# Kernel optimization log

Measured on AMD Instinct MI355X. Metric: run time of the kernel, lower is better.

Reference implementation:

```python
import jax, jax.numpy as jnp
import numpy as np


def setup_inputs() -> dict:
    key = jax.random.key(0)
    ks = jax.random.split(key, 9)
    B, S, D, E, I = 4, 2048, 1024, 8, 2048
    sd = 1.0 / np.sqrt(D)
    si = 1.0 / np.sqrt(I)
    return {
        "hidden_states": jax.random.normal(ks[0], (B, S, D), dtype=jnp.float32),
        "gate_w": jax.random.normal(ks[1], (D, E), dtype=jnp.float32) * sd,
        "expert_gate_w": jax.random.normal(ks[2], (E, D, I), dtype=jnp.float32) * sd,
        "expert_up_w": jax.random.normal(ks[3], (E, D, I), dtype=jnp.float32) * sd,
        "expert_down_w": jax.random.normal(ks[4], (E, I, D), dtype=jnp.float32) * si,
        "shared_gate_proj_w": jax.random.normal(ks[5], (D, I), dtype=jnp.float32) * sd,
        "shared_up_w": jax.random.normal(ks[6], (D, I), dtype=jnp.float32) * sd,
        "shared_down_w": jax.random.normal(ks[7], (I, D), dtype=jnp.float32) * si,
        "shared_expert_gate_w": jax.random.normal(ks[8], (D, 1), dtype=jnp.float32) * sd,
        "top_k": 2,
    }


def reference(hidden_states, gate_w, expert_gate_w, expert_up_w, expert_down_w,
              shared_gate_proj_w, shared_up_w, shared_down_w, shared_expert_gate_w,
              top_k):
    B, S, D = hidden_states.shape
    E = gate_w.shape[1]
    x = hidden_states.reshape(-1, D)            # [T, D]
    T = x.shape[0]

    # Router: softmax in fp32, top-k, dense per-token per-expert combine weights.
    gate_vals = x @ gate_w                      # [T, E]
    probs = jax.nn.softmax(gate_vals.astype(jnp.float32), axis=-1)
    top_w, top_i = jax.lax.top_k(probs, top_k)  # [T, K]
    dense_w = jnp.zeros((T, E), dtype=jnp.float32)
    dense_w = dense_w.at[jnp.arange(T)[:, None], top_i].set(top_w)
    dense_w = dense_w.astype(x.dtype)           # zero for unselected experts

    # All experts as batched SwiGLU GEMMs (tokens with zero weight contribute 0).
    g = jnp.einsum('td,edi->eti', x, expert_gate_w)
    u = jnp.einsum('td,edi->eti', x, expert_up_w)
    y = jnp.einsum('eti,eid->etd', jax.nn.silu(g) * u, expert_down_w)  # [E, T, D]
    moe_out = jnp.einsum('etd,te->td', y, dense_w)                      # [T, D]

    # Shared expert with sigmoid gate.
    shared = (jax.nn.silu(x @ shared_gate_proj_w) * (x @ shared_up_w)) @ shared_down_w
    shared = jax.nn.sigmoid(x @ shared_expert_gate_w) * shared

    final = (moe_out + shared).reshape(B, S, D)
    return final, gate_vals
```

## Files before the change

kernel.cpp:

```cpp
#include <hip/hip_runtime.h>

typedef __bf16 bf16x8 __attribute__((ext_vector_type(8)));
typedef float f32x4 __attribute__((ext_vector_type(4)));
typedef float f4 __attribute__((ext_vector_type(4)));
typedef unsigned short us8 __attribute__((ext_vector_type(8)));

#define T_TOK 8192
#define DDIM 1024
#define NEXP 8
#define IDIM 2048
#define NCH 1024
#define RROWS 17408
#define ROWS_TOT (T_TOK + RROWS)

__device__ __forceinline__ unsigned short f2bf(float f) {
    unsigned u = __float_as_uint(f);
    u += 0x7fffu + ((u >> 16) & 1u);
    return (unsigned short)(u >> 16);
}

#define GLDS(src, dst) __builtin_amdgcn_global_load_lds( \
    (const __attribute__((address_space(1))) void*)(src), \
    (__attribute__((address_space(3))) void*)(dst), 16, 0, 0)

__global__ __launch_bounds__(256) void router_kernel(
    const float* __restrict__ x, const float* __restrict__ gate_w,
    const float* __restrict__ sgw, float* __restrict__ gate_out,
    float* __restrict__ wdense, float* __restrict__ sgout)
{
    __shared__ float lgw[DDIM * NEXP];
    __shared__ float lsg[DDIM];
    int tid = threadIdx.x;
    for (int i = tid; i < (DDIM * NEXP) / 4; i += 256)
        ((f4*)lgw)[i] = ((const f4*)gate_w)[i];
    for (int i = tid; i < DDIM / 4; i += 256)
        ((f4*)lsg)[i] = ((const f4*)sgw)[i];
    __syncthreads();

    int wid = tid >> 6, l = tid & 63;
    int t = blockIdx.x * 4 + wid;

    float acc[NEXP];
#pragma unroll
    for (int e = 0; e < NEXP; e++) acc[e] = 0.f;
    float accs = 0.f;
    const float* xr = x + (size_t)t * DDIM;
#pragma unroll
    for (int j = 0; j < 4; j++) {
        int d0 = j * 256 + l * 4;
        f4 xv = *(const f4*)(xr + d0);
#pragma unroll
        for (int c = 0; c < 4; c++) {
            float xd = xv[c];
            int d = d0 + c;
#pragma unroll
            for (int e = 0; e < NEXP; e++) acc[e] += xd * lgw[d * NEXP + e];
            accs += xd * lsg[d];
        }
    }
#pragma unroll
    for (int off = 32; off > 0; off >>= 1) {
#pragma unroll
        for (int e = 0; e < NEXP; e++) acc[e] += __shfl_xor(acc[e], off);
        accs += __shfl_xor(accs, off);
    }
    if (l == 0) {
        float m = acc[0];
        for (int e = 1; e < NEXP; e++) m = fmaxf(m, acc[e]);
        float p[NEXP], s = 0.f;
        for (int e = 0; e < NEXP; e++) { p[e] = __expf(acc[e] - m); s += p[e]; }
        float inv = 1.f / s;
        int i1 = 0; float b1 = p[0];
        for (int e = 1; e < NEXP; e++) if (p[e] > b1) { b1 = p[e]; i1 = e; }
        int i2 = -1; float b2 = -1.f;
        for (int e = 0; e < NEXP; e++) if (e != i1 && p[e] > b2) { b2 = p[e]; i2 = e; }
        for (int e = 0; e < NEXP; e++) {
            gate_out[(size_t)t * NEXP + e] = acc[e];
            float w = (e == i1) ? b1 * inv : (e == i2) ? b2 * inv : 0.f;
            wdense[(size_t)t * NEXP + e] = w;
        }
        sgout[t] = 1.f / (1.f + __expf(-accs));
    }
}

__global__ __launch_bounds__(256) void bucket_kernel(
    const float* __restrict__ wdense, int* __restrict__ list,
    float* __restrict__ wl, int* __restrict__ cnt,
    int* __restrict__ te, int* __restrict__ tp)
{
    int e = blockIdx.x;
    int tid = threadIdx.x, wid = tid >> 6, l = tid & 63;
    __shared__ int wsum[4];
    int base = 0;
    int* le = list + (size_t)e * T_TOK;
    float* we = wl + (size_t)e * T_TOK;
    for (int t0 = 0; t0 < T_TOK; t0 += 256) {
        int tok = t0 + tid;
        float w = wdense[(size_t)tok * NEXP + e];
        bool f = w > 0.f;
        unsigned long long m = __ballot(f);
        int lp = __popcll(m & ((1ull << l) - 1ull));
        if (l == 0) wsum[wid] = __popcll(m);
        __syncthreads();
        int woff = 0;
#pragma unroll
        for (int i = 0; i < 4; i++) if (i < wid) woff += wsum[i];
        int btot = wsum[0] + wsum[1] + wsum[2] + wsum[3];
        if (f) {
            int pos = base + woff + lp;
            le[pos] = tok; we[pos] = w;
            int slot = 0;
            for (int e2 = 0; e2 < e; e2++)
                slot += (wdense[(size_t)tok * NEXP + e2] > 0.f) ? 1 : 0;
            te[tok * 2 + slot] = e;
            tp[tok * 2 + slot] = pos;
        }
        base += btot;
        __syncthreads();
    }
    if (tid == 0) cnt[e] = base;
    int align = (base + 255) & ~255;
    for (int i = base + tid; i < align; i += 256) { le[i] = 0; we[i] = 0.f; }
}

__global__ void scan_kernel(const int* __restrict__ cnt, int* __restrict__ offs)
{
    if (threadIdx.x == 0) {
        int o = 0;
        for (int e = 0; e < NEXP; e++) { offs[e] = o; o += (cnt[e] + 127) & ~127; }
    }
}

__global__ __launch_bounds__(256) void cvt_kernel(
    const float* __restrict__ in, unsigned short* __restrict__ out, int n8)
{
    int i = blockIdx.x * 256 + threadIdx.x;
    if (i >= n8) return;
    const f4* p = (const f4*)in + (size_t)i * 2;
    f4 a = p[0], b = p[1];
    us8 o;
#pragma unroll
    for (int k = 0; k < 4; k++) { o[k] = f2bf(a[k]); o[4 + k] = f2bf(b[k]); }
    *((us8*)out + i) = o;
}

__global__ __launch_bounds__(256) void wcvt_gu_kernel(
    const float* __restrict__ egw, const float* __restrict__ euw,
    const float* __restrict__ sgp, const float* __restrict__ sup,
    unsigned short* __restrict__ pool, int c0)
{
    int j = blockIdx.y;
    int e = j >> 1, s = j & 1;
    const float* src = (e < 8) ? ((s ? euw : egw) + (size_t)e * DDIM * IDIM)
                               : (s ? sup : sgp);
    unsigned short* dst = pool + (size_t)j * NCH * DDIM;
    int tpc = NCH / 64;
    int tci = blockIdx.x % tpc, tri = blockIdx.x / tpc;
    int r0 = tri * 64;
    int cl0 = tci * 64;
    int cg0 = c0 + cl0;

    __shared__ unsigned short lds[64][72];
    int t = threadIdx.x;
    int tr = t >> 4, tcc = (t & 15) * 4;
#pragma unroll
    for (int jj = 0; jj < 4; jj++) {
        int r = tr + jj * 16;
        f4 v = *(const f4*)(src + (size_t)(r0 + r) * IDIM + cg0 + tcc);
#pragma unroll
        for (int k = 0; k < 4; k++) lds[r][tcc + k] = f2bf(v[k]);
    }
    __syncthreads();
    int orow = t >> 2, ss = t & 3;
    us8 v0, v1;
#pragma unroll
    for (int i = 0; i < 8; i++) {
        v0[i] = lds[ss * 16 + i][orow];
        v1[i] = lds[ss * 16 + 8 + i][orow];
    }
    unsigned short* op = dst + (size_t)(cl0 + orow) * DDIM + r0 + ss * 16;
    *(us8*)op = v0; *(us8*)(op + 8) = v1;
}

__global__ __launch_bounds__(256) void wcvt_d_kernel(
    const float* __restrict__ edw, const float* __restrict__ sdw,
    unsigned short* __restrict__ pool)
{
    int j = blockIdx.y;
    const float* src = (j < 8) ? edw + (size_t)j * IDIM * DDIM : sdw;
    unsigned short* dst = pool + (size_t)j * DDIM * IDIM;
    int tpc = DDIM / 64;
    int tci = blockIdx.x % tpc, tri = blockIdx.x / tpc;
    int rg0 = tri * 64;
    int cg0 = tci * 64;

    __shared__ unsigned short lds[64][72];
    int t = threadIdx.x;
    int tr = t >> 4, tcc = (t & 15) * 4;
#pragma unroll
    for (int jj = 0; jj < 4; jj++) {
        int r = tr + jj * 16;
        f4 v = *(const f4*)(src + (size_t)(rg0 + r) * DDIM + cg0 + tcc);
#pragma unroll
        for (int k = 0; k < 4; k++) lds[r][tcc + k] = f2bf(v[k]);
    }
    __syncthreads();
    int orow = t >> 2, ss = t & 3;
    us8 v0, v1;
#pragma unroll
    for (int i = 0; i < 8; i++) {
        v0[i] = lds[ss * 16 + i][orow];
        v1[i] = lds[ss * 16 + 8 + i][orow];
    }
    unsigned short* op = dst + (size_t)(cg0 + orow) * IDIM + rg0 + ss * 16;
    *(us8*)op = v0; *(us8*)(op + 8) = v1;
}

__global__ __launch_bounds__(512, 1) void gemm_gateup8(
    const unsigned short* __restrict__ A, const unsigned short* __restrict__ pool,
    unsigned short* __restrict__ H, const int* __restrict__ listb,
    const int* __restrict__ cnt, const int* __restrict__ offs, int c0)
{
    int z = blockIdx.z;
    const unsigned short *Bg, *Bu; const int* lst; int count, rowb;
    if (z == 0) {
        Bg = pool + (size_t)16 * NCH * DDIM; Bu = pool + (size_t)17 * NCH * DDIM;
        lst = nullptr; count = T_TOK; rowb = 0;
    } else {
        int e = z - 1;
        Bg = pool + (size_t)(e * 2) * NCH * DDIM; Bu = pool + (size_t)(e * 2 + 1) * NCH * DDIM;
        lst = listb + (size_t)e * T_TOK; count = cnt[e]; rowb = T_TOK + offs[e];
    }
    int m0 = blockIdx.y * 256, n0 = blockIdx.x * 128;
    if (m0 >= count) return;
    int climit = (count + 127) & ~127;
    const int NT = DDIM / 64;

    __shared__ unsigned short lds[2][32768];

    int tid = threadIdx.x, wid = tid >> 6, l = tid & 63;
    int wm = wid >> 1, wn = wid & 1;
    int lr = l & 15, lkg = l >> 4;

    int sb = tid & 7, sr = tid >> 3;
    int sk = (sb ^ (sr & 7)) << 3;
    const unsigned short* pa[2][2];
#pragma unroll
    for (int h = 0; h < 2; h++)
#pragma unroll
        for (int j = 0; j < 2; j++) {
            int rr = m0 + h * 128 + j * 64 + sr;
            int ga = lst ? lst[rr] : rr;
            pa[h][j] = A + (size_t)ga * DDIM + sk;
        }
    const unsigned short* pbg = Bg + (size_t)(n0 + sr) * DDIM + sk;
    const unsigned short* pbu = Bu + (size_t)(n0 + sr) * DDIM + sk;

#define GU_ST_A(sbuf, h, t) { \
    GLDS(pa[h][0] + (t) * 64, (sbuf) + (h) * 8192 + tid * 8); \
    GLDS(pa[h][1] + (t) * 64, (sbuf) + (h) * 8192 + 4096 + tid * 8); }
#define GU_ST_BG(sbuf, t) { \
    GLDS(pbg + (t) * 64, (sbuf) + 16384 + tid * 8); \
    GLDS(pbg + (size_t)64 * DDIM + (t) * 64, (sbuf) + 16384 + 4096 + tid * 8); }
#define GU_ST_BU(sbuf, t) { \
    GLDS(pbu + (t) * 64, (sbuf) + 24576 + tid * 8); \
    GLDS(pbu + (size_t)64 * DDIM + (t) * 64, (sbuf) + 24576 + 4096 + tid * 8); }

    {
        unsigned short* s0 = &lds[0][0];
        GU_ST_A(s0, 0, 0); GU_ST_A(s0, 1, 0); GU_ST_BG(s0, 0); GU_ST_BU(s0, 0);
        unsigned short* s1 = &lds[1][0];
        GU_ST_A(s1, 0, 1); GU_ST_A(s1, 1, 1); GU_ST_BG(s1, 1); GU_ST_BU(s1, 1);
    }

    int xorc = (lr & 7) << 3;
    int kx0 = (lkg * 8) ^ xorc;
    int kx1 = (32 + lkg * 8) ^ xorc;
    int aoff[4], boff[4];
#pragma unroll
    for (int mf = 0; mf < 4; mf++) {
        int r = wm * 64 + mf * 16 + lr;
        aoff[mf] = (r >> 7) * 8192 + (r & 127) * 64;
    }
#pragma unroll
    for (int nf = 0; nf < 4; nf++)
        boff[nf] = 16384 + (wn * 64 + nf * 16 + lr) * 64;

    f32x4 zero = {0.f, 0.f, 0.f, 0.f};
    f32x4 accg[4][4], accu[4][4];
#pragma unroll
    for (int m = 0; m < 4; m++)
#pragma unroll
        for (int n = 0; n < 4; n++) { accg[m][n] = zero; accu[m][n] = zero; }

    bf16x8 a[2][2], bg[4][2], bu[4][2];

#pragma unroll 1
    for (int t = 0; t < NT; t++) {
        const unsigned short* cb = &lds[t & 1][0];
        unsigned short* sbuf = &lds[t & 1][0];
        bool stg = (t + 2 < NT);

        if (t == NT - 1) { asm volatile("s_waitcnt vmcnt(0)" ::: "memory"); }
        else             { asm volatile("s_waitcnt vmcnt(8)" ::: "memory"); }
        __builtin_amdgcn_s_barrier();
#pragma unroll
        for (int mf = 0; mf < 2; mf++) {
            a[mf][0] = *(const bf16x8*)(cb + aoff[mf] + kx0);
            a[mf][1] = *(const bf16x8*)(cb + aoff[mf] + kx1);
        }
#pragma unroll
        for (int nf = 0; nf < 2; nf++) {
            bg[nf][0] = *(const bf16x8*)(cb + boff[nf] + kx0);
            bg[nf][1] = *(const bf16x8*)(cb + boff[nf] + kx1);
            bu[nf][0] = *(const bf16x8*)(cb + boff[nf] + 8192 + kx0);
            bu[nf][1] = *(const bf16x8*)(cb + boff[nf] + 8192 + kx1);
        }
        __builtin_amdgcn_s_setprio(1);
#pragma unroll
        for (int kh = 0; kh < 2; kh++)
#pragma unroll
            for (int mf = 0; mf < 2; mf++)
#pragma unroll
                for (int nf = 0; nf < 2; nf++) {
                    accg[mf][nf] = __builtin_amdgcn_mfma_f32_16x16x32_bf16(a[mf][kh], bg[nf][kh], accg[mf][nf], 0, 0, 0);
                    accu[mf][nf] = __builtin_amdgcn_mfma_f32_16x16x32_bf16(a[mf][kh], bu[nf][kh], accu[mf][nf], 0, 0, 0);
                }
        __builtin_amdgcn_s_setprio(0);

        __builtin_amdgcn_s_barrier();
#pragma unroll
        for (int nf = 2; nf < 4; nf++) {
            bg[nf][0] = *(const bf16x8*)(cb + boff[nf] + kx0);
            bg[nf][1] = *(const bf16x8*)(cb + boff[nf] + kx1);
            bu[nf][0] = *(const bf16x8*)(cb + boff[nf] + 8192 + kx0);
            bu[nf][1] = *(const bf16x8*)(cb + boff[nf] + 8192 + kx1);
        }
        __builtin_amdgcn_s_setprio(1);
#pragma unroll
        for (int kh = 0; kh < 2; kh++)
#pragma unroll
            for (int mf = 0; mf < 2; mf++)
#pragma unroll
                for (int nf = 2; nf < 4; nf++) {
                    accg[mf][nf] = __builtin_amdgcn_mfma_f32_16x16x32_bf16(a[mf][kh], bg[nf][kh], accg[mf][nf], 0, 0, 0);
                    accu[mf][nf] = __builtin_amdgcn_mfma_f32_16x16x32_bf16(a[mf][kh], bu[nf][kh], accu[mf][nf], 0, 0, 0);
                }
        __builtin_amdgcn_s_setprio(0);

        __builtin_amdgcn_s_barrier();
#pragma unroll
        for (int mf = 0; mf < 2; mf++) {
            a[mf][0] = *(const bf16x8*)(cb + aoff[2 + mf] + kx0);
            a[mf][1] = *(const bf16x8*)(cb + aoff[2 + mf] + kx1);
        }
        if (stg) { GU_ST_BG(sbuf, t + 2); }
        __builtin_amdgcn_s_setprio(1);
#pragma unroll
        for (int kh = 0; kh < 2; kh++)
#pragma unroll
            for (int mf = 0; mf < 2; mf++)
#pragma unroll
                for (int nf = 0; nf < 2; nf++) {
                    accg[2 + mf][nf] = __builtin_amdgcn_mfma_f32_16x16x32_bf16(a[mf][kh], bg[nf][kh], accg[2 + mf][nf], 0, 0, 0);
                    accu[2 + mf][nf] = __builtin_amdgcn_mfma_f32_16x16x32_bf16(a[mf][kh], bu[nf][kh], accu[2 + mf][nf], 0, 0, 0);
                }
        __builtin_amdgcn_s_setprio(0);

        __builtin_amdgcn_s_barrier();
        if (stg) { GU_ST_BU(sbuf, t + 2); GU_ST_A(sbuf, 0, t + 2); GU_ST_A(sbuf, 1, t + 2); }
        __builtin_amdgcn_s_setprio(1);
#pragma unroll
        for (int kh = 0; kh < 2; kh++)
#pragma unroll
            for (int mf = 0; mf < 2; mf++)
#pragma unroll
                for (int nf = 2; nf < 4; nf++) {
                    accg[2 + mf][nf] = __builtin_amdgcn_mfma_f32_16x16x32_bf16(a[mf][kh], bg[nf][kh], accg[2 + mf][nf], 0, 0, 0);
                    accu[2 + mf][nf] = __builtin_amdgcn_mfma_f32_16x16x32_bf16(a[mf][kh], bu[nf][kh], accu[2 + mf][nf], 0, 0, 0);
                }
        __builtin_amdgcn_s_setprio(0);
    }

#pragma unroll
    for (int mf = 0; mf < 4; mf++) {
        int rbase = m0 + wm * 64 + mf * 16 + lkg * 4;
#pragma unroll
        for (int nf = 0; nf < 4; nf++) {
            int col = c0 + n0 + wn * 64 + nf * 16 + lr;
#pragma unroll
            for (int r = 0; r < 4; r++) {
                int rloc = rbase + r;
                if (rloc < climit) {
                    float g = accg[mf][nf][r], u = accu[mf][nf][r];
                    float hv = g * (1.f / (1.f + __expf(-g))) * u;
                    H[(size_t)(rowb + rloc) * IDIM + col] = f2bf(hv);
                }
            }
        }
    }
}

__global__ __launch_bounds__(512, 1) void gemm_down8(
    const unsigned short* __restrict__ H, const unsigned short* __restrict__ pool,
    unsigned short* __restrict__ Y,
    const float* __restrict__ wlb, const float* __restrict__ sgo,
    const int* __restrict__ cnt, const int* __restrict__ offs)
{
    int z = blockIdx.z;
    const unsigned short* B; const float* coef; int count, rowb;
    if (z == 0) {
        B = pool + (size_t)8 * DDIM * IDIM;
        coef = sgo; count = T_TOK; rowb = 0;
    } else {
        int e = z - 1;
        B = pool + (size_t)e * DDIM * IDIM;
        coef = wlb + (size_t)e * T_TOK;
        count = cnt[e]; rowb = T_TOK + offs[e];
    }
    int m0 = blockIdx.y * 128, n0 = blockIdx.x * 256;
    if (m0 >= count) return;
    int climit = (count + 127) & ~127;
    const int NT = IDIM / 64;

    __shared__ unsigned short lds[2][24576];

    int tid = threadIdx.x, wid = tid >> 6, l = tid & 63;
    int wm = wid >> 2, wn = wid & 3;
    int lr = l & 15, lkg = l >> 4;

    int sr = tid >> 3;
    int sk = ((tid & 7) ^ (sr & 7)) << 3;
    const unsigned short* pah = H + (size_t)(rowb + m0 + sr) * IDIM + sk;
    const unsigned short* pb  = B + (size_t)(n0 + sr) * IDIM + sk;

#define DN_ST(sbuf, t) { \
    GLDS(pah + (t) * 64, (sbuf) + tid * 8); \
    GLDS(pah + (size_t)64 * IDIM + (t) * 64, (sbuf) + 4096 + tid * 8); \
    GLDS(pb + (t) * 64, (sbuf) + 8192 + tid * 8); \
    GLDS(pb + (size_t)64 * IDIM + (t) * 64, (sbuf) + 8192 + 4096 + tid * 8); \
    GLDS(pb + (size_t)128 * IDIM + (t) * 64, (sbuf) + 16384 + tid * 8); \
    GLDS(pb + (size_t)192 * IDIM + (t) * 64, (sbuf) + 16384 + 4096 + tid * 8); }

    {
        unsigned short* s0 = &lds[0][0];
        DN_ST(s0, 0);
        unsigned short* s1 = &lds[1][0];
        DN_ST(s1, 1);
    }

    int xorc = (lr & 7) << 3;
    int kx0 = (lkg * 8) ^ xorc;
    int kx1 = (32 + lkg * 8) ^ xorc;
    int aoff[4], boff[4];
#pragma unroll
    for (int mf = 0; mf < 4; mf++)
        aoff[mf] = (wm * 64 + mf * 16 + lr) * 64;
#pragma unroll
    for (int nf = 0; nf < 4; nf++)
        boff[nf] = 8192 + (wn * 64 + nf * 16 + lr) * 64;

    f32x4 zero = {0.f, 0.f, 0.f, 0.f};
    f32x4 acc[4][4];
#pragma unroll
    for (int m = 0; m < 4; m++)
#pragma unroll
        for (int n = 0; n < 4; n++) acc[m][n] = zero;

    bf16x8 a[4][2], b[4][2];

#pragma unroll 1
    for (int t = 0; t < NT; t++) {
        const unsigned short* cb = &lds[t & 1][0];
        unsigned short* sbuf = &lds[t & 1][0];
        bool stg = (t + 2 < NT);

        if (t == NT - 1) { asm volatile("s_waitcnt vmcnt(0)" ::: "memory"); }
        else             { asm volatile("s_waitcnt vmcnt(6)" ::: "memory"); }
        __builtin_amdgcn_s_barrier();
#pragma unroll
        for (int mf = 0; mf < 4; mf++) {
            a[mf][0] = *(const bf16x8*)(cb + aoff[mf] + kx0);
            a[mf][1] = *(const bf16x8*)(cb + aoff[mf] + kx1);
        }
#pragma unroll
        for (int nf = 0; nf < 4; nf++) {
            b[nf][0] = *(const bf16x8*)(cb + boff[nf] + kx0);
            b[nf][1] = *(const bf16x8*)(cb + boff[nf] + kx1);
        }
        __builtin_amdgcn_s_setprio(1);
#pragma unroll
        for (int kh = 0; kh < 2; kh++)
#pragma unroll
            for (int mf = 0; mf < 4; mf++)
#pragma unroll
                for (int nf = 0; nf < 2; nf++)
                    acc[mf][nf] = __builtin_amdgcn_mfma_f32_16x16x32_bf16(a[mf][kh], b[nf][kh], acc[mf][nf], 0, 0, 0);
        __builtin_amdgcn_s_setprio(0);

        __builtin_amdgcn_s_barrier();
        if (stg) { DN_ST(sbuf, t + 2); }
        __builtin_amdgcn_s_setprio(1);
#pragma unroll
        for (int kh = 0; kh < 2; kh++)
#pragma unroll
            for (int mf = 0; mf < 4; mf++)
#pragma unroll
                for (int nf = 2; nf < 4; nf++)
                    acc[mf][nf] = __builtin_amdgcn_mfma_f32_16x16x32_bf16(a[mf][kh], b[nf][kh], acc[mf][nf], 0, 0, 0);
        __builtin_amdgcn_s_setprio(0);
    }

#pragma unroll
    for (int mf = 0; mf < 4; mf++) {
        int rbase = m0 + wm * 64 + mf * 16 + lkg * 4;
        float cf[4];
#pragma unroll
        for (int r = 0; r < 4; r++) {
            int rloc = rbase + r;
            cf[r] = (rloc < climit) ? coef[rloc] : 0.f;
        }
#pragma unroll
        for (int nf = 0; nf < 4; nf++) {
            int col = n0 + wn * 64 + nf * 16 + lr;
#pragma unroll
            for (int r = 0; r < 4; r++) {
                int rloc = rbase + r;
                if (rloc < climit)
                    Y[(size_t)(rowb + rloc) * DDIM + col] = f2bf(cf[r] * acc[mf][nf][r]);
            }
        }
    }
}

__global__ __launch_bounds__(256) void combine_kernel(
    const unsigned short* __restrict__ Y, const int* __restrict__ te,
    const int* __restrict__ tp, const int* __restrict__ offs,
    float* __restrict__ out)
{
    int t = blockIdx.x * 2 + (threadIdx.x >> 7);
    int c = (threadIdx.x & 127) * 8;
    int e0 = te[2 * t], e1 = te[2 * t + 1];
    size_t r0 = (size_t)T_TOK + offs[e0] + tp[2 * t];
    size_t r1 = (size_t)T_TOK + offs[e1] + tp[2 * t + 1];

    us8 vs = *(const us8*)(Y + (size_t)t * DDIM + c);
    us8 v0 = *(const us8*)(Y + r0 * DDIM + c);
    us8 v1 = *(const us8*)(Y + r1 * DDIM + c);
    f4 o0, o1;
#pragma unroll
    for (int k = 0; k < 4; k++) {
        o0[k] = __uint_as_float((unsigned)vs[k] << 16)
              + __uint_as_float((unsigned)v0[k] << 16)
              + __uint_as_float((unsigned)v1[k] << 16);
        o1[k] = __uint_as_float((unsigned)vs[4 + k] << 16)
              + __uint_as_float((unsigned)v0[4 + k] << 16)
              + __uint_as_float((unsigned)v1[4 + k] << 16);
    }
    float* op = out + (size_t)t * DDIM + c;
    *(f4*)op = o0;
    *(f4*)(op + 4) = o1;
}

extern "C" void kernel_launch(void* const* d_in, const int* in_sizes, int n_in,
                              void* d_out, int out_size, void* d_ws, size_t ws_size,
                              hipStream_t stream)
{
    const float* x   = (const float*)d_in[0];
    const float* gw  = (const float*)d_in[1];
    const float* egw = (const float*)d_in[2];
    const float* euw = (const float*)d_in[3];
    const float* edw = (const float*)d_in[4];
    const float* sgp = (const float*)d_in[5];
    const float* sup = (const float*)d_in[6];
    const float* sdw = (const float*)d_in[7];
    const float* seg = (const float*)d_in[8];

    float* out0 = (float*)d_out;
    float* gate_out = out0 + (size_t)T_TOK * DDIM;

    char* ws = (char*)d_ws;
    auto take = [&](size_t bytes) { char* p = ws; ws += (bytes + 255) & ~(size_t)255; return p; };
    unsigned short* xb   = (unsigned short*)take((size_t)T_TOK * DDIM * 2);
    float* wdense = (float*)take((size_t)T_TOK * NEXP * 4);
    float* sgo    = (float*)take((size_t)T_TOK * 4);
    int*   list   = (int*)take((size_t)NEXP * T_TOK * 4);
    float* wl     = (float*)take((size_t)NEXP * T_TOK * 4);
    int*   cnt    = (int*)take(256);
    int*   offs   = (int*)take(256);
    int*   te     = (int*)take((size_t)T_TOK * 2 * 4);
    int*   tp     = (int*)take((size_t)T_TOK * 2 * 4);
    unsigned short* pool = (unsigned short*)take((size_t)18 * NCH * DDIM * 2);
    unsigned short* H    = (unsigned short*)take((size_t)ROWS_TOT * IDIM * 2);
    unsigned short* Y    = (unsigned short*)take((size_t)ROWS_TOT * DDIM * 2);

    router_kernel<<<T_TOK / 4, 256, 0, stream>>>(x, gw, seg, gate_out, wdense, sgo);
    bucket_kernel<<<NEXP, 256, 0, stream>>>(wdense, list, wl, cnt, te, tp);
    scan_kernel<<<1, 64, 0, stream>>>(cnt, offs);
    cvt_kernel<<<(T_TOK * DDIM / 8) / 256, 256, 0, stream>>>(x, xb, T_TOK * DDIM / 8);

    for (int c = 0; c < 2; c++) {
        int c0 = c * NCH;
        wcvt_gu_kernel<<<dim3((NCH / 64) * 16, 18), 256, 0, stream>>>(
            egw, euw, sgp, sup, pool, c0);
        gemm_gateup8<<<dim3(NCH / 128, T_TOK / 256, 9), 512, 0, stream>>>(
            xb, pool, H, list, cnt, offs, c0);
    }

    wcvt_d_kernel<<<dim3((IDIM / 64) * 16, 9), 256, 0, stream>>>(edw, sdw, pool);
    gemm_down8<<<dim3(DDIM / 256, T_TOK / 128, 9), 512, 0, stream>>>(
        H, pool, Y, wl, sgo, cnt, offs);

    combine_kernel<<<T_TOK / 2, 256, 0, stream>>>(Y, te, tp, offs, out0);
}
```

Baseline: 574.8 us.

## Pre-swizzle down-proj weights into MFMA fragment layout and load B directly to registers

The down-projection weight conversion now writes bf16 weights in an MFMA-fragment-major layout, so each lane reads its B fragment with one contiguous 16-byte global load. gemm_down8 drops B from LDS and instead double-buffers B fragments in registers, prefetched one K step ahead. Only the A tile is staged in LDS. The block shrinks to 256 threads with a 128x128 tile and occupancy 2, and gemm_gateup8's launch bound also asks for 2 blocks per CU. The aim is to cut LDS traffic and footprint and raise occupancy, at the cost of more register pressure and uncoalesced-by-tile global B reads that rely on L2 reuse.

After: 598.6 us. +4.1%, slower.

```diff
diff --git a/kernel.cpp b/kernel.cpp
--- a/kernel.cpp
+++ b/kernel.cpp
@@ -189,12 +189,11 @@
     int j = blockIdx.y;
     const float* src = (j < 8) ? edw + (size_t)j * IDIM * DDIM : sdw;
     unsigned short* dst = pool + (size_t)j * DDIM * IDIM;
-    int tpc = DDIM / 64;
-    int tci = blockIdx.x % tpc, tri = blockIdx.x / tpc;
+    int tci = blockIdx.x & 15, tri = blockIdx.x >> 4;
     int rg0 = tri * 64;
     int cg0 = tci * 64;
 
-    __shared__ unsigned short lds[64][72];
+    __shared__ unsigned short lt[64][72];
     int t = threadIdx.x;
     int tr = t >> 4, tcc = (t & 15) * 4;
 #pragma unroll
@@ -202,21 +201,23 @@
         int r = tr + jj * 16;
         f4 v = *(const f4*)(src + (size_t)(rg0 + r) * DDIM + cg0 + tcc);
 #pragma unroll
-        for (int k = 0; k < 4; k++) lds[r][tcc + k] = f2bf(v[k]);
+        for (int k = 0; k < 4; k++) lt[tcc + k][r] = f2bf(v[k]);
     }
     __syncthreads();
-    int orow = t >> 2, ss = t & 3;
-    us8 v0, v1;
-#pragma unroll
-    for (int i = 0; i < 8; i++) {
-        v0[i] = lds[ss * 16 + i][orow];
-        v1[i] = lds[ss * 16 + 8 + i][orow];
-    }
-    unsigned short* op = dst + (size_t)(cg0 + orow) * IDIM + rg0 + ss * 16;
-    *(us8*)op = v0; *(us8*)(op + 8) = v1;
-}
-
-__global__ __launch_bounds__(512, 1) void gemm_gateup8(
+#pragma unroll
+    for (int c2 = 0; c2 < 2; c2++) {
+        int c = t + 256 * c2;
+        int frag = c >> 6, lane = c & 63;
+        int nfl = frag >> 1, kfl = frag & 1;
+        int n_l = nfl * 16 + (lane & 15);
+        int k_l = kfl * 32 + ((lane >> 4) * 8);
+        us8 v = *(const us8*)(&lt[n_l][k_l]);
+        int nf = tci * 4 + nfl, kf = tri * 2 + kfl;
+        *(us8*)(dst + ((size_t)(nf * 64 + kf) * 64 + lane) * 8) = v;
+    }
+}
+
+__global__ __launch_bounds__(512, 2) void gemm_gateup8(
     const unsigned short* __restrict__ A, const unsigned short* __restrict__ pool,
     unsigned short* __restrict__ H, const int* __restrict__ listb,
     const int* __restrict__ cnt, const int* __restrict__ offs, int c0)
@@ -401,7 +402,7 @@
     }
 }
 
-__global__ __launch_bounds__(512, 1) void gemm_down8(
+__global__ __launch_bounds__(256, 2) void gemm_down8(
     const unsigned short* __restrict__ H, const unsigned short* __restrict__ pool,
     unsigned short* __restrict__ Y,
     const float* __restrict__ wlb, const float* __restrict__ sgo,
@@ -418,47 +419,44 @@
         coef = wlb + (size_t)e * T_TOK;
         count = cnt[e]; rowb = T_TOK + offs[e];
     }
-    int m0 = blockIdx.y * 128, n0 = blockIdx.x * 256;
+    int m0 = blockIdx.y * 128, n0 = blockIdx.x * 128;
     if (m0 >= count) return;
     int climit = (count + 127) & ~127;
     const int NT = IDIM / 64;
 
-    __shared__ unsigned short lds[2][24576];
+    __shared__ unsigned short lds[2][8192];
 
     int tid = threadIdx.x, wid = tid >> 6, l = tid & 63;
-    int wm = wid >> 2, wn = wid & 3;
+    int wm = wid >> 1, wn = wid & 1;
     int lr = l & 15, lkg = l >> 4;
 
     int sr = tid >> 3;
     int sk = ((tid & 7) ^ (sr & 7)) << 3;
-    const unsigned short* pah = H + (size_t)(rowb + m0 + sr) * IDIM + sk;
-    const unsigned short* pb  = B + (size_t)(n0 + sr) * IDIM + sk;
-
-#define DN_ST(sbuf, t) { \
-    GLDS(pah + (t) * 64, (sbuf) + tid * 8); \
-    GLDS(pah + (size_t)64 * IDIM + (t) * 64, (sbuf) + 4096 + tid * 8); \
-    GLDS(pb + (t) * 64, (sbuf) + 8192 + tid * 8); \
-    GLDS(pb + (size_t)64 * IDIM + (t) * 64, (sbuf) + 8192 + 4096 + tid * 8); \
-    GLDS(pb + (size_t)128 * IDIM + (t) * 64, (sbuf) + 16384 + tid * 8); \
-    GLDS(pb + (size_t)192 * IDIM + (t) * 64, (sbuf) + 16384 + 4096 + tid * 8); }
-
-    {
-        unsigned short* s0 = &lds[0][0];
-        DN_ST(s0, 0);
-        unsigned short* s1 = &lds[1][0];
-        DN_ST(s1, 1);
+    const unsigned short* pa0 = H + (size_t)(rowb + m0 + sr) * IDIM + sk;
+    const unsigned short* pa1 = H + (size_t)(rowb + m0 + sr + 32) * IDIM + sk;
+    const unsigned short* pa2 = H + (size_t)(rowb + m0 + sr + 64) * IDIM + sk;
+    const unsigned short* pa3 = H + (size_t)(rowb + m0 + sr + 96) * IDIM + sk;
+
+#define DN_STAGE(SB, tt) { \
+    GLDS(pa0 + (size_t)(tt) * 64, (SB) + tid * 8); \
+    GLDS(pa1 + (size_t)(tt) * 64, (SB) + 2048 + tid * 8); \
+    GLDS(pa2 + (size_t)(tt) * 64, (SB) + 4096 + tid * 8); \
+    GLDS(pa3 + (size_t)(tt) * 64, (SB) + 6144 + tid * 8); }
+
+    const unsigned short* bb[4];
+#pragma unroll
+    for (int f = 0; f < 4; f++) {
+        int nf = blockIdx.x * 8 + wn * 4 + f;
+        bb[f] = B + (size_t)nf * 32768 + (size_t)l * 8;
     }
 
     int xorc = (lr & 7) << 3;
-    int kx0 = (lkg * 8) ^ xorc;
-    int kx1 = (32 + lkg * 8) ^ xorc;
-    int aoff[4], boff[4];
+    int kxx0 = (lkg * 8) ^ xorc;
+    int kxx1 = (32 + lkg * 8) ^ xorc;
+    int aoff[4];
 #pragma unroll
     for (int mf = 0; mf < 4; mf++)
         aoff[mf] = (wm * 64 + mf * 16 + lr) * 64;
-#pragma unroll
-    for (int nf = 0; nf < 4; nf++)
-        boff[nf] = 8192 + (wn * 64 + nf * 16 + lr) * 64;
 
     f32x4 zero = {0.f, 0.f, 0.f, 0.f};
     f32x4 acc[4][4];
@@ -467,48 +465,59 @@
 #pragma unroll
         for (int n = 0; n < 4; n++) acc[m][n] = zero;
 
-    bf16x8 a[4][2], b[4][2];
+    bf16x8 brA[4][2], brB[4][2];
+
+    DN_STAGE(&lds[0][0], 0);
+    DN_STAGE(&lds[1][0], 1);
+#pragma unroll
+    for (int f = 0; f < 4; f++) {
+        brA[f][0] = *(const bf16x8*)(bb[f]);
+        brA[f][1] = *(const bf16x8*)(bb[f] + 512);
+    }
+    __builtin_amdgcn_sched_barrier(0);
+    asm volatile("s_waitcnt vmcnt(12)" ::: "memory");
+    __builtin_amdgcn_s_barrier();
+
+#define DN_BODY(T, CB, BRCUR, BRNXT) { \
+    bool bnext = (T) + 1 < NT; \
+    bool stg = (T) + 2 < NT; \
+    if (bnext) { \
+        int kf2 = ((T) + 1) * 2; \
+        _Pragma("unroll") \
+        for (int f = 0; f < 4; f++) { \
+            BRNXT[f][0] = *(const bf16x8*)(bb[f] + (size_t)kf2 * 512); \
+            BRNXT[f][1] = *(const bf16x8*)(bb[f] + (size_t)(kf2 + 1) * 512); \
+        } \
+    } \
+    __builtin_amdgcn_sched_barrier(0); \
+    bf16x8 a_[4][2]; \
+    _Pragma("unroll") \
+    for (int mf = 0; mf < 4; mf++) { \
+        a_[mf][0] = *(const bf16x8*)((CB) + aoff[mf] + kxx0); \
+        a_[mf][1] = *(const bf16x8*)((CB) + aoff[mf] + kxx1); \
+    } \
+    __builtin_amdgcn_s_setprio(1); \
+    _Pragma("unroll") \
+    for (int kh = 0; kh < 2; kh++) \
+        _Pragma("unroll") \
+        for (int mf = 0; mf < 4; mf++) \
+            _Pragma("unroll") \
+            for (int nf = 0; nf < 4; nf++) \
+                acc[mf][nf] = __builtin_amdgcn_mfma_f32_16x16x32_bf16(a_[mf][kh], BRCUR[nf][kh], acc[mf][nf], 0, 0, 0); \
+    __builtin_amdgcn_s_setprio(0); \
+    __builtin_amdgcn_s_barrier(); \
+    if (stg) { DN_STAGE((CB), (T) + 2); } \
+    __builtin_amdgcn_sched_barrier(0); \
+    if (bnext && stg)      { asm volatile("s_waitcnt vmcnt(12)" ::: "memory"); } \
+    else if (bnext)        { asm volatile("s_waitcnt vmcnt(8)" ::: "memory"); } \
+    else                   { asm volatile("s_waitcnt vmcnt(0)" ::: "memory"); } \
+    __builtin_amdgcn_s_barrier(); \
+}
 
 #pragma unroll 1
-    for (int t = 0; t < NT; t++) {
-        const unsigned short* cb = &lds[t & 1][0];
-        unsigned short* sbuf = &lds[t & 1][0];
-        bool stg = (t + 2 < NT);
-
-        if (t == NT - 1) { asm volatile("s_waitcnt vmcnt(0)" ::: "memory"); }
-        else             { asm volatile("s_waitcnt vmcnt(6)" ::: "memory"); }
-        __builtin_amdgcn_s_barrier();
-#pragma unroll
-        for (int mf = 0; mf < 4; mf++) {
-            a[mf][0] = *(const bf16x8*)(cb + aoff[mf] + kx0);
-            a[mf][1] = *(const bf16x8*)(cb + aoff[mf] + kx1);
-        }
-#pragma unroll
-        for (int nf = 0; nf < 4; nf++) {
-            b[nf][0] = *(const bf16x8*)(cb + boff[nf] + kx0);
-            b[nf][1] = *(const bf16x8*)(cb + boff[nf] + kx1);
-        }
-        __builtin_amdgcn_s_setprio(1);
-#pragma unroll
-        for (int kh = 0; kh < 2; kh++)
-#pragma unroll
-            for (int mf = 0; mf < 4; mf++)
-#pragma unroll
-                for (int nf = 0; nf < 2; nf++)
-                    acc[mf][nf] = __builtin_amdgcn_mfma_f32_16x16x32_bf16(a[mf][kh], b[nf][kh], acc[mf][nf], 0, 0, 0);
-        __builtin_amdgcn_s_setprio(0);
-
-        __builtin_amdgcn_s_barrier();
-        if (stg) { DN_ST(sbuf, t + 2); }
-        __builtin_amdgcn_s_setprio(1);
-#pragma unroll
-        for (int kh = 0; kh < 2; kh++)
-#pragma unroll
-            for (int mf = 0; mf < 4; mf++)
-#pragma unroll
-                for (int nf = 2; nf < 4; nf++)
-                    acc[mf][nf] = __builtin_amdgcn_mfma_f32_16x16x32_bf16(a[mf][kh], b[nf][kh], acc[mf][nf], 0, 0, 0);
-        __builtin_amdgcn_s_setprio(0);
+    for (int t = 0; t < NT; t += 2) {
+        DN_BODY(t,     &lds[0][0], brA, brB);
+        DN_BODY(t + 1, &lds[1][0], brB, brA);
     }
 
 #pragma unroll
@@ -607,8 +616,8 @@
             xb, pool, H, list, cnt, offs, c0);
     }
 
-    wcvt_d_kernel<<<dim3((IDIM / 64) * 16, 9), 256, 0, stream>>>(edw, sdw, pool);
-    gemm_down8<<<dim3(DDIM / 256, T_TOK / 128, 9), 512, 0, stream>>>(
+    wcvt_d_kernel<<<dim3(512, 9), 256, 0, stream>>>(edw, sdw, pool);
+    gemm_down8<<<dim3(DDIM / 128, T_TOK / 128, 9), 256, 0, stream>>>(
         H, pool, Y, wl, sgo, cnt, offs);
 
     combine_kernel<<<T_TOK / 2, 256, 0, stream>>>(Y, te, tp, offs, out0);
```
